# Optimization experiments

Hardware: AMD Instinct MI355X
Metric: run time of the kernel (lower is better)

Reference implementation:

```python
import jax, jax.numpy as jnp
import numpy as np

EPS = 1e-5  # nn.LayerNorm default
H = 16      # n_heads

def _ln(x, s, b):
    m = x.mean(-1, keepdims=True)
    v = x.var(-1, keepdims=True)
    return (x - m) / jnp.sqrt(v + EPS) * s + b


def setup_inputs() -> dict:
    key = jax.random.key(0)
    B, T, D, L, V = 2, 1024, 1024, 6, 32000
    ks = jax.random.split(key, 10)
    def n(k, shape):
        return jax.random.normal(k, shape, dtype=jnp.float32) * 0.02
    return dict(
        x=jax.random.randint(ks[0], (B, T), 0, V),
        tok_emb=n(ks[1], (V, D)),
        pos_emb=n(ks[2], (T, D)),
        Wq=n(ks[3], (L, D, D)), bq=jnp.zeros((L, D), jnp.float32),
        Wk=n(ks[4], (L, D, D)), bk=jnp.zeros((L, D), jnp.float32),
        Wv=n(ks[5], (L, D, D)), bv=jnp.zeros((L, D), jnp.float32),
        ln1_s=jnp.ones((L, D), jnp.float32), ln1_b=jnp.zeros((L, D), jnp.float32),
        W1=n(ks[6], (L, D, 4 * D)), b1=jnp.zeros((L, 4 * D), jnp.float32),
        W2=n(ks[7], (L, 4 * D, D)), b2=jnp.zeros((L, D), jnp.float32),
        ln2_s=jnp.ones((L, D), jnp.float32), ln2_b=jnp.zeros((L, D), jnp.float32),
        Wout=n(ks[8], (D, V)), bout=jnp.zeros((V,), jnp.float32),
    )


def reference(x, tok_emb, pos_emb, Wq, bq, Wk, bk, Wv, bv, ln1_s, ln1_b,
              W1, b1, W2, b2, ln2_s, ln2_b, Wout, bout):
    B, T = x.shape
    D = tok_emb.shape[1]
    hd = D // H
    # embeddings (dropout = identity in eval)
    h = tok_emb[x] + pos_emb[:T]
    # additive causal mask: +1.0 on allowed (tril ones kept), -inf elsewhere,
    # exactly matching torch's tril-ones masked_fill mask
    tril = jnp.tril(jnp.ones((T, T), dtype=h.dtype))
    mask = jnp.where(tril == 0, -jnp.inf, 1.0).astype(h.dtype)
    scale = jnp.asarray(1.0 / np.sqrt(hd), h.dtype)

    def block(h, p):
        wq, bq_, wk, bk_, wv, bv_, l1s, l1b, w1, b1_, w2, b2_, l2s, l2b = p
        def heads(W, b):  # [B,T,D] -> [B,H,T,hd]
            return (h @ W + b).reshape(B, T, H, hd).transpose(0, 2, 1, 3)
        q, k, v = heads(wq, bq_), heads(wk, bk_), heads(wv, bv_)
        s = jnp.einsum('bhqd,bhkd->bhqk', q, k) * scale + mask
        a = jax.nn.softmax(s, axis=-1)
        o = jnp.einsum('bhqk,bhkd->bhqd', a, v).transpose(0, 2, 1, 3).reshape(B, T, D)
        hi = _ln(o + h, l1s, l1b)
        f = jax.nn.relu(hi @ w1 + b1_) @ w2 + b2_
        return _ln(f + hi, l2s, l2b), None

    h, _ = jax.lax.scan(block, h, (Wq, bq, Wk, bk, Wv, bv, ln1_s, ln1_b,
                                   W1, b1, W2, b2, ln2_s, ln2_b))
    return h @ Wout + bout
```

## Files before the change

### kernel.cpp

```cpp
#include <hip/hip_runtime.h>
#include <cstdint>
#include <cstddef>

typedef short bf16x8 __attribute__((ext_vector_type(8)));
typedef float f32x4 __attribute__((ext_vector_type(4)));
typedef unsigned short us4 __attribute__((ext_vector_type(4)));

#define DEV static __device__ __forceinline__

DEV unsigned short f2bf(float f) {
  union { float f; unsigned u; } v; v.f = f;
  unsigned r = v.u + 0x7FFFu + ((v.u >> 16) & 1u);
  return (unsigned short)(r >> 16);
}

DEV void gll16(const void* g, void* l) {
  __builtin_amdgcn_global_load_lds((const __attribute__((address_space(1))) void*)g,
                                   (__attribute__((address_space(3))) void*)l,
                                   16, 0, 0);
}

__global__ __launch_bounds__(256) void embed_kernel(
    const int* __restrict__ x, const float* __restrict__ te,
    const float* __restrict__ pe, float* __restrict__ hf,
    unsigned short* __restrict__ hb) {
  int row = blockIdx.x;
  int t = row & 1023;
  int tok = x[row];
  int tid = threadIdx.x;
  float4 v = ((const float4*)(te + (size_t)tok * 1024))[tid];
  float4 p = ((const float4*)(pe + (size_t)t * 1024))[tid];
  v.x += p.x; v.y += p.y; v.z += p.z; v.w += p.w;
  ((float4*)(hf + (size_t)row * 1024))[tid] = v;
  us4 bv; bv[0] = f2bf(v.x); bv[1] = f2bf(v.y); bv[2] = f2bf(v.z); bv[3] = f2bf(v.w);
  ((us4*)(hb + (size_t)row * 1024))[tid] = bv;
}

__global__ __launch_bounds__(256) void wconv_kernel(
    const float* __restrict__ W, unsigned short* __restrict__ Wt, int K, int N) {
  __shared__ float tile[32][33];
  int n0 = blockIdx.x * 32, k0 = blockIdx.y * 32;
  int tx = threadIdx.x & 31, ty = threadIdx.x >> 5;
#pragma unroll
  for (int i = 0; i < 4; ++i)
    tile[ty * 4 + i][tx] = W[(size_t)(k0 + ty * 4 + i) * N + n0 + tx];
  __syncthreads();
#pragma unroll
  for (int i = 0; i < 4; ++i)
    Wt[(size_t)(n0 + ty * 4 + i) * K + k0 + tx] = f2bf(tile[tx][ty * 4 + i]);
}

__global__ __launch_bounds__(256) void wconv5_kernel(
    const float* __restrict__ Wqf, const float* __restrict__ Wkf,
    const float* __restrict__ Wvf, const float* __restrict__ W1f,
    const float* __restrict__ W2f, unsigned short* __restrict__ wsc) {
  __shared__ float tile[32][33];
  const int bid = blockIdx.x;
  const float* W; unsigned short* Wt; int K, N, b;
  if (bid < 3072) {
    const int s = bid >> 10; b = bid & 1023;
    W = s == 0 ? Wqf : (s == 1 ? Wkf : Wvf);
    Wt = wsc + (size_t)s * 1048576; K = 1024; N = 1024;
  } else if (bid < 7168) {
    b = bid - 3072; W = W1f; Wt = wsc + 3145728; K = 1024; N = 4096;
  } else {
    b = bid - 7168; W = W2f; Wt = wsc + 7340032; K = 4096; N = 1024;
  }
  const int nb = N >> 5;
  const int n0 = (b & (nb - 1)) * 32, k0 = (b / nb) * 32;
  const int tx = threadIdx.x & 31, ty = threadIdx.x >> 5;
#pragma unroll
  for (int i = 0; i < 4; ++i)
    tile[ty * 4 + i][tx] = W[(size_t)(k0 + ty * 4 + i) * N + n0 + tx];
  __syncthreads();
#pragma unroll
  for (int i = 0; i < 4; ++i)
    Wt[(size_t)(n0 + ty * 4 + i) * K + k0 + tx] = f2bf(tile[tx][ty * 4 + i]);
}

template <int EPI>
__global__ __launch_bounds__(512) void gemm5_kernel(
    const unsigned short* __restrict__ A, const unsigned short* __restrict__ Bt,
    const float* __restrict__ bias1, const float* __restrict__ bias2,
    const float* __restrict__ bias3, void* __restrict__ C1,
    void* __restrict__ C2, void* __restrict__ C3,
    int M, int N, int Kstride, int klen, int nbm) {
  constexpr int BM = 256, BN = 128, BK = 64;
  __shared__ unsigned short lA[BM * BK];
  __shared__ unsigned short lB[BN * BK];
  const int tid = threadIdx.x;
  const int wid = tid >> 6, lane = tid & 63;
  const int g = lane >> 4, c = lane & 15;
  const int wm = wid >> 1, wn = wid & 1;

  const int nwg = gridDim.x;
  const int q = nwg >> 3, r = nwg & 7;
  const int xcd = blockIdx.x & 7, jj = blockIdx.x >> 3;
  const int wgid = (xcd < r) ? (xcd * (q + 1) + jj)
                             : (r * (q + 1) + (xcd - r) * q + jj);
  const int bm = (wgid % nbm) * BM;
  const int bn = (wgid / nbm) * BN;
  const int k0 = blockIdx.z * klen;

  f32x4 acc[4][4];
#pragma unroll
  for (int mi = 0; mi < 4; ++mi)
#pragma unroll
    for (int ni = 0; ni < 4; ++ni) acc[mi][ni] = f32x4{0.f, 0.f, 0.f, 0.f};

  for (int kb = 0; kb < klen; kb += BK) {
#pragma unroll
    for (int it = 0; it < 4; ++it) {
      int chunk = it * 512 + tid;
      int row = chunk >> 3, cr = chunk & 7;
      int sc = cr ^ (row & 7);
      gll16(A + (size_t)(bm + row) * Kstride + k0 + kb + sc * 8,
            lA + (size_t)(it * 512 + wid * 64) * 8);
    }
#pragma unroll
    for (int it = 0; it < 2; ++it) {
      int chunk = it * 512 + tid;
      int row = chunk >> 3, cr = chunk & 7;
      int sc = cr ^ (row & 7);
      gll16(Bt + (size_t)(bn + row) * Kstride + k0 + kb + sc * 8,
            lB + (size_t)(it * 512 + wid * 64) * 8);
    }
    __syncthreads();
#pragma unroll
    for (int kk = 0; kk < 2; ++kk) {
      bf16x8 af[4], bfr[4];
#pragma unroll
      for (int mi = 0; mi < 4; ++mi) {
        int row = wm * 64 + mi * 16 + c;
        int ch = (kk * 4 + g) ^ (row & 7);
        af[mi] = *(const bf16x8*)(lA + row * BK + ch * 8);
      }
#pragma unroll
      for (int ni = 0; ni < 4; ++ni) {
        int row = wn * 64 + ni * 16 + c;
        int ch = (kk * 4 + g) ^ (row & 7);
        bfr[ni] = *(const bf16x8*)(lB + row * BK + ch * 8);
      }
#pragma unroll
      for (int mi = 0; mi < 4; ++mi)
#pragma unroll
        for (int ni = 0; ni < 4; ++ni)
          acc[mi][ni] = __builtin_amdgcn_mfma_f32_16x16x32_bf16(
              af[mi], bfr[ni], acc[mi][ni], 0, 0, 0);
    }
    __syncthreads();
  }

  const bool z0 = (blockIdx.z == 0);
#pragma unroll
  for (int mi = 0; mi < 4; ++mi) {
    const int row0 = bm + wm * 64 + mi * 16 + g * 4;
#pragma unroll
    for (int ni = 0; ni < 4; ++ni) {
      const int col = bn + wn * 64 + ni * 16 + c;
      if constexpr (EPI == 0) {
        float* C = (float*)C1 + (size_t)blockIdx.z * M * N;
        const float bv = z0 ? bias1[col] : 0.f;
#pragma unroll
        for (int rr = 0; rr < 4; ++rr)
          C[(size_t)(row0 + rr) * N + col] = acc[mi][ni][rr] + bv;
      } else if constexpr (EPI == 2) {
        const float bv = bias1[col];
#pragma unroll
        for (int rr = 0; rr < 4; ++rr)
          ((unsigned short*)C1)[(size_t)(row0 + rr) * N + col] =
              f2bf(fmaxf(acc[mi][ni][rr] + bv, 0.f));
      } else {
        if (col < 1024) {
          const float bv = bias1[col];
#pragma unroll
          for (int rr = 0; rr < 4; ++rr)
            ((unsigned short*)C1)[(size_t)(row0 + rr) * 1024 + col] =
                f2bf(acc[mi][ni][rr] + bv);
        } else if (col < 2048) {
          const float bv = bias2[col - 1024];
#pragma unroll
          for (int rr = 0; rr < 4; ++rr)
            ((unsigned short*)C2)[(size_t)(row0 + rr) * 1024 + (col - 1024)] =
                f2bf(acc[mi][ni][rr] + bv);
        } else {
          const int cp = col - 2048;
          const float bv = bias3[cp];
          const int hh = cp >> 6, hd = cp & 63;
#pragma unroll
          for (int rr = 0; rr < 4; ++rr) {
            const int row = row0 + rr;
            const int b = row >> 10, t = row & 1023;
            ((unsigned short*)C3)[(size_t)((b * 16 + hh) * 64 + hd) * 1024 + t] =
                f2bf(acc[mi][ni][rr] + bv);
          }
        }
      }
    }
  }
}

__global__ __launch_bounds__(256) void attn_kernel(
    const unsigned short* __restrict__ q, const unsigned short* __restrict__ k,
    const unsigned short* __restrict__ vt, float* __restrict__ o) {
  __shared__ unsigned short lK[128 * 64];
  __shared__ unsigned short lV[64 * 128];
  __shared__ unsigned short lP[4][16 * 128];
  const int tid = threadIdx.x, wid = tid >> 6, lane = tid & 63;
  const int g = lane >> 4, c = lane & 15;
  const int qb = blockIdx.x * 64;
  const int h = blockIdx.y;
  const int b = blockIdx.z;
  const int qw = qb + wid * 16;

  bf16x8 aq[2];
#pragma unroll
  for (int kk = 0; kk < 2; ++kk)
    aq[kk] = *(const bf16x8*)(q + (size_t)(b * 1024 + qw + c) * 1024 + h * 64 + kk * 32 + g * 8);

  float m_run[4], l_run[4];
  f32x4 acc_o[4];
#pragma unroll
  for (int rr = 0; rr < 4; ++rr) { m_run[rr] = -INFINITY; l_run[rr] = 0.f; }
#pragma unroll
  for (int ni = 0; ni < 4; ++ni) acc_o[ni] = f32x4{0.f, 0.f, 0.f, 0.f};

  const int ntiles = (qb >> 7) + 1;
  for (int kt = 0; kt < ntiles; ++kt) {
#pragma unroll
    for (int it = 0; it < 4; ++it) {
      int chunk = it * 256 + tid;
      int row = chunk >> 3, cr = chunk & 7;
      int sc = cr ^ (row & 7);
      gll16(k + (size_t)(b * 1024 + kt * 128 + row) * 1024 + h * 64 + sc * 8,
            lK + (size_t)(it * 256 + wid * 64) * 8);
    }
#pragma unroll
    for (int it = 0; it < 4; ++it) {
      int chunk = it * 256 + tid;
      int row = chunk >> 4, cr = chunk & 15;
      int sc = cr ^ (row & 7);
      gll16(vt + (size_t)((b * 16 + h) * 64 + row) * 1024 + kt * 128 + sc * 8,
            lV + (size_t)(it * 256 + wid * 64) * 8);
    }
    __syncthreads();

    f32x4 accs[8];
#pragma unroll
    for (int ni = 0; ni < 8; ++ni) accs[ni] = f32x4{0.f, 0.f, 0.f, 0.f};
    __builtin_amdgcn_s_setprio(1);
#pragma unroll
    for (int kk = 0; kk < 2; ++kk)
#pragma unroll
      for (int ni = 0; ni < 8; ++ni) {
        int row = ni * 16 + c;
        int ch = (kk * 4 + g) ^ (row & 7);
        bf16x8 kf = *(const bf16x8*)(lK + row * 64 + ch * 8);
        accs[ni] = __builtin_amdgcn_mfma_f32_16x16x32_bf16(aq[kk], kf, accs[ni], 0, 0, 0);
      }
    __builtin_amdgcn_s_setprio(0);

    const bool diag = (kt == ntiles - 1);
    float p[8][4], rowmax[4];
#pragma unroll
    for (int rr = 0; rr < 4; ++rr) rowmax[rr] = -INFINITY;
#pragma unroll
    for (int ni = 0; ni < 8; ++ni)
#pragma unroll
      for (int rr = 0; rr < 4; ++rr) {
        float s = accs[ni][rr] * 0.125f;
        if (diag) {
          int ktok = kt * 128 + ni * 16 + c;
          int qtok = qw + g * 4 + rr;
          if (ktok > qtok) s = -INFINITY;
        }
        p[ni][rr] = s;
        rowmax[rr] = fmaxf(rowmax[rr], s);
      }
#pragma unroll
    for (int mm = 1; mm < 16; mm <<= 1)
#pragma unroll
      for (int rr = 0; rr < 4; ++rr)
        rowmax[rr] = fmaxf(rowmax[rr], __shfl_xor(rowmax[rr], mm, 64));

    float alpha[4];
#pragma unroll
    for (int rr = 0; rr < 4; ++rr) {
      float mn = fmaxf(m_run[rr], rowmax[rr]);
      alpha[rr] = __expf(m_run[rr] - mn);
      m_run[rr] = mn;
    }
#pragma unroll
    for (int ni = 0; ni < 8; ++ni)
#pragma unroll
      for (int rr = 0; rr < 4; ++rr) p[ni][rr] = __expf(p[ni][rr] - m_run[rr]);

    float rowsum[4];
#pragma unroll
    for (int rr = 0; rr < 4; ++rr)
      rowsum[rr] = ((p[0][rr] + p[1][rr]) + (p[2][rr] + p[3][rr])) +
                   ((p[4][rr] + p[5][rr]) + (p[6][rr] + p[7][rr]));
#pragma unroll
    for (int mm = 1; mm < 16; mm <<= 1)
#pragma unroll
      for (int rr = 0; rr < 4; ++rr) rowsum[rr] += __shfl_xor(rowsum[rr], mm, 64);
#pragma unroll
    for (int rr = 0; rr < 4; ++rr) l_run[rr] = l_run[rr] * alpha[rr] + rowsum[rr];
#pragma unroll
    for (int ni = 0; ni < 4; ++ni)
#pragma unroll
      for (int rr = 0; rr < 4; ++rr) acc_o[ni][rr] *= alpha[rr];

#pragma unroll
    for (int ni = 0; ni < 8; ++ni)
#pragma unroll
      for (int rr = 0; rr < 4; ++rr) {
        int qrow = g * 4 + rr;
        int tok = ni * 16 + c;
        int ch = (tok >> 3) ^ (qrow & 7);
        lP[wid][qrow * 128 + ch * 8 + (tok & 7)] = f2bf(p[ni][rr]);
      }

    __builtin_amdgcn_s_setprio(1);
#pragma unroll
    for (int kk = 0; kk < 4; ++kk) {
      int kc = kk * 4 + g;
      int chp = kc ^ (c & 7);
      bf16x8 pa = *(const bf16x8*)(&lP[wid][c * 128 + chp * 8]);
#pragma unroll
      for (int ni = 0; ni < 4; ++ni) {
        int row = ni * 16 + c;
        int ch = kc ^ (row & 7);
        bf16x8 vf = *(const bf16x8*)(lV + row * 128 + ch * 8);
        acc_o[ni] = __builtin_amdgcn_mfma_f32_16x16x32_bf16(pa, vf, acc_o[ni], 0, 0, 0);
      }
    }
    __builtin_amdgcn_s_setprio(0);
    __syncthreads();
  }

#pragma unroll
  for (int ni = 0; ni < 4; ++ni)
#pragma unroll
    for (int rr = 0; rr < 4; ++rr) {
      int row = b * 1024 + qw + g * 4 + rr;
      int col = h * 64 + ni * 16 + c;
      o[(size_t)row * 1024 + col] = acc_o[ni][rr] / l_run[rr];
    }
}

template <int NP>
__global__ __launch_bounds__(256) void ln_add_kernel(
    const float* __restrict__ a1, const float* __restrict__ res,
    const float* __restrict__ s, const float* __restrict__ bb,
    float* __restrict__ out_f, unsigned short* __restrict__ out_b) {
  int row = blockIdx.x, tid = threadIdx.x;
  float4 x = ((const float4*)(a1 + (size_t)row * 1024))[tid];
  float4 rv = ((const float4*)(res + (size_t)row * 1024))[tid];
  x.x += rv.x; x.y += rv.y; x.z += rv.z; x.w += rv.w;
#pragma unroll
  for (int pimg = 1; pimg < NP; ++pimg) {
    float4 x2 = ((const float4*)(a1 + (size_t)pimg * 2097152 + (size_t)row * 1024))[tid];
    x.x += x2.x; x.y += x2.y; x.z += x2.z; x.w += x2.w;
  }
  float sum = x.x + x.y + x.z + x.w;
  float sq = x.x * x.x + x.y * x.y + x.z * x.z + x.w * x.w;
#pragma unroll
  for (int mm = 1; mm < 64; mm <<= 1) {
    sum += __shfl_xor(sum, mm, 64);
    sq += __shfl_xor(sq, mm, 64);
  }
  __shared__ float ssum[4], ssq[4];
  int wid = tid >> 6, lane = tid & 63;
  if (lane == 0) { ssum[wid] = sum; ssq[wid] = sq; }
  __syncthreads();
  sum = ssum[0] + ssum[1] + ssum[2] + ssum[3];
  sq = ssq[0] + ssq[1] + ssq[2] + ssq[3];
  float mean = sum * (1.f / 1024.f);
  float var = sq * (1.f / 1024.f) - mean * mean;
  float rstd = rsqrtf(var + 1e-5f);
  float4 sv = ((const float4*)s)[tid];
  float4 bv = ((const float4*)bb)[tid];
  float4 y;
  y.x = (x.x - mean) * rstd * sv.x + bv.x;
  y.y = (x.y - mean) * rstd * sv.y + bv.y;
  y.z = (x.z - mean) * rstd * sv.z + bv.z;
  y.w = (x.w - mean) * rstd * sv.w + bv.w;
  ((float4*)(out_f + (size_t)row * 1024))[tid] = y;
  us4 ob; ob[0] = f2bf(y.x); ob[1] = f2bf(y.y); ob[2] = f2bf(y.z); ob[3] = f2bf(y.w);
  ((us4*)(out_b + (size_t)row * 1024))[tid] = ob;
}

extern "C" void kernel_launch(void* const* d_in, const int* in_sizes, int n_in,
                              void* d_out, int out_size, void* d_ws, size_t ws_size,
                              hipStream_t stream) {
  const int D = 1024, DFF = 4096, V = 32000, L = 6;
  const int* x = (const int*)d_in[0];
  const float* tok_emb = (const float*)d_in[1];
  const float* pos_emb = (const float*)d_in[2];
  const float* Wq = (const float*)d_in[3];  const float* bq = (const float*)d_in[4];
  const float* Wk = (const float*)d_in[5];  const float* bk = (const float*)d_in[6];
  const float* Wv = (const float*)d_in[7];  const float* bv = (const float*)d_in[8];
  const float* ln1s = (const float*)d_in[9];  const float* ln1b = (const float*)d_in[10];
  const float* W1 = (const float*)d_in[11];  const float* b1 = (const float*)d_in[12];
  const float* W2 = (const float*)d_in[13];  const float* b2 = (const float*)d_in[14];
  const float* ln2s = (const float*)d_in[15]; const float* ln2b = (const float*)d_in[16];
  const float* Wout = (const float*)d_in[17]; const float* bout = (const float*)d_in[18];

  char* ws = (char*)d_ws;
  float* h_res = (float*)(ws + 0);
  float* hi_res = (float*)(ws + 8388608);
  float* tmp = (float*)(ws + 16777216);
  unsigned short* hbf = (unsigned short*)(ws + 25165824);
  unsigned short* qb_ = (unsigned short*)(ws + 29360128);
  unsigned short* kb_ = (unsigned short*)(ws + 33554432);
  unsigned short* vtb = (unsigned short*)(ws + 37748736);
  unsigned short* ffn1 = (unsigned short*)(ws + 41943040);
  unsigned short* wsc = (unsigned short*)(ws + 58720256);
  float* part = (float*)(ws + 58720256 + 25165824);

  embed_kernel<<<2048, 256, 0, stream>>>(x, tok_emb, pos_emb, h_res, hbf);

  for (int l = 0; l < L; ++l) {
    wconv5_kernel<<<11264, 256, 0, stream>>>(
        Wq + (size_t)l * D * D, Wk + (size_t)l * D * D, Wv + (size_t)l * D * D,
        W1 + (size_t)l * D * DFF, W2 + (size_t)l * DFF * D, wsc);
    gemm5_kernel<4><<<192, 512, 0, stream>>>(
        hbf, wsc, bq + l * D, bk + l * D, bv + l * D, qb_, kb_, vtb,
        2048, 3072, D, D, 8);
    attn_kernel<<<dim3(16, 16, 2), 256, 0, stream>>>(qb_, kb_, vtb, tmp);
    ln_add_kernel<1><<<2048, 256, 0, stream>>>(
        tmp, h_res, ln1s + l * D, ln1b + l * D, hi_res, hbf);
    gemm5_kernel<2><<<256, 512, 0, stream>>>(
        hbf, wsc + 3145728, b1 + l * DFF, nullptr, nullptr, ffn1, nullptr, nullptr,
        2048, DFF, D, D, 8);
    gemm5_kernel<0><<<dim3(64, 1, 4), 512, 0, stream>>>(
        ffn1, wsc + 7340032, b2 + l * D, nullptr, nullptr, part, nullptr, nullptr,
        2048, D, DFF, 1024, 8);
    ln_add_kernel<4><<<2048, 256, 0, stream>>>(
        part, hi_res, ln2s + l * D, ln2b + l * D, h_res, hbf);
  }

  wconv_kernel<<<dim3(1000, 32), 256, 0, stream>>>(Wout, wsc, D, V);
  gemm5_kernel<0><<<2000, 512, 0, stream>>>(
      hbf, wsc, bout, nullptr, nullptr, (float*)d_out, nullptr, nullptr,
      2048, V, D, D, 8);
}
```

Before: 1.155 ms.

## Add 256x256 ping-pong GEMM with XCD remap for output projection

Adds a new GEMM kernel with 256x256 tiles, double-buffered LDS loaded via global_load_lds in half-tile stages interleaved with four MFMA quadrants, explicit vmcnt waits and barriers, setprio around MFMA bursts, and an XCD-aware workgroup remapping. It replaces the previous gemm5 launch for the final vocab projection (2048x32000x1024). Larger tiles raise arithmetic intensity and the staged schedule aims to overlap loads with MFMA, at the cost of one workgroup per CU and many barriers.

```diff
diff --git a/kernel.cpp b/kernel.cpp
--- a/kernel.cpp
+++ b/kernel.cpp
@@ -19,6 +19,15 @@
                                    (__attribute__((address_space(3))) void*)l,
                                    16, 0, 0);
 }
+
+template <int N> DEV void waitvm() {
+  if constexpr (N == 0) asm volatile("s_waitcnt vmcnt(0)" ::: "memory");
+  else if constexpr (N == 6) asm volatile("s_waitcnt vmcnt(6)" ::: "memory");
+  else asm volatile("s_waitcnt vmcnt(8)" ::: "memory");
+}
+
+#define SB0 __builtin_amdgcn_sched_barrier(0)
+#define BARR do { SB0; __builtin_amdgcn_s_barrier(); SB0; } while (0)
 
 __global__ __launch_bounds__(256) void embed_kernel(
     const int* __restrict__ x, const float* __restrict__ te,
@@ -198,6 +207,159 @@
       }
     }
   }
+}
+
+template <int BM, int BN, int EPI>
+__global__ __launch_bounds__(512, 1) void gemm8_kernel(
+    const unsigned short* __restrict__ A, const unsigned short* __restrict__ Bt,
+    const float* __restrict__ bias1, void* __restrict__ C1,
+    int M, int N, int K, int nbm) {
+  constexpr int BK = 64;
+  constexpr int MFR = BM / 64;
+  constexpr int NFR = BN / 128;
+  constexpr int IA = BM / 128;
+  constexpr int IB = BN / 128;
+  constexpr int VMW = IA + 2 * IB;
+  __shared__ unsigned short lA[2 * BM * BK];
+  __shared__ unsigned short lB[2 * BN * BK];
+  const int tid = threadIdx.x, wid = tid >> 6, lane = tid & 63;
+  const int g = lane >> 4, c = lane & 15;
+  const int wm = wid >> 2, wn = wid & 3;
+
+  const int nwg = gridDim.x;
+  const int q = nwg >> 3, r = nwg & 7;
+  const int xcd = blockIdx.x & 7, jj = blockIdx.x >> 3;
+  const int wgid = (xcd < r) ? (xcd * (q + 1) + jj)
+                             : (r * (q + 1) + (xcd - r) * q + jj);
+  const int bm = (wgid % nbm) * BM;
+  const int bn = (wgid / nbm) * BN;
+  const int NT = K / BK;
+
+  f32x4 acc[2][MFR][2][NFR];
+#pragma unroll
+  for (int a = 0; a < 2; ++a)
+#pragma unroll
+    for (int mi = 0; mi < MFR; ++mi)
+#pragma unroll
+      for (int b = 0; b < 2; ++b)
+#pragma unroll
+        for (int ni = 0; ni < NFR; ++ni) acc[a][mi][b][ni] = f32x4{0.f, 0.f, 0.f, 0.f};
+
+  bf16x8 af[2][MFR][2];
+  bf16x8 bfr[2][NFR][2];
+
+#define STG_A(tileI, half) do {                                              \
+    const int t_ = (tileI);                                                  \
+    const int kb_ = (t_ < NT ? t_ : NT - 1) * BK;                            \
+    unsigned short* dA_ = lA + (t_ & 1) * (BM * BK);                         \
+    _Pragma("unroll")                                                        \
+    for (int i_ = 0; i_ < IA; ++i_) {                                        \
+      const int chunk_ = (half) * (BM * 4) + i_ * 512 + tid;                 \
+      const int row_ = chunk_ >> 3, cr_ = chunk_ & 7;                        \
+      const int sc_ = cr_ ^ (row_ & 7);                                      \
+      gll16(A + (size_t)(bm + row_) * K + kb_ + sc_ * 8,                     \
+            dA_ + ((half) * (BM * 4) + i_ * 512 + wid * 64) * 8);            \
+    } } while (0)
+
+#define STG_B(tileI, half) do {                                              \
+    const int t_ = (tileI);                                                  \
+    const int kb_ = (t_ < NT ? t_ : NT - 1) * BK;                            \
+    unsigned short* dB_ = lB + (t_ & 1) * (BN * BK);                         \
+    _Pragma("unroll")                                                        \
+    for (int i_ = 0; i_ < IB; ++i_) {                                        \
+      const int chunk_ = (half) * (BN * 4) + i_ * 512 + tid;                 \
+      const int row_ = chunk_ >> 3, cr_ = chunk_ & 7;                        \
+      const int sc_ = cr_ ^ (row_ & 7);                                      \
+      gll16(Bt + (size_t)(bn + row_) * K + kb_ + sc_ * 8,                    \
+            dB_ + ((half) * (BN * 4) + i_ * 512 + wid * 64) * 8);            \
+    } } while (0)
+
+#define RD_A(qm_) do {                                                       \
+    const unsigned short* sA_ = lA + cur * (BM * BK);                        \
+    _Pragma("unroll")                                                        \
+    for (int mi = 0; mi < MFR; ++mi)                                         \
+      _Pragma("unroll")                                                      \
+      for (int kk = 0; kk < 2; ++kk) {                                       \
+        const int row_ = (qm_) * (BM / 2) + wm * (BM / 4) + mi * 16 + c;     \
+        const int ch_ = (kk * 4 + g) ^ (row_ & 7);                           \
+        af[qm_][mi][kk] = *(const bf16x8*)(sA_ + row_ * BK + ch_ * 8);       \
+      } } while (0)
+
+#define RD_B(qn_) do {                                                       \
+    const unsigned short* sB_ = lB + cur * (BN * BK);                        \
+    _Pragma("unroll")                                                        \
+    for (int ni = 0; ni < NFR; ++ni)                                         \
+      _Pragma("unroll")                                                      \
+      for (int kk = 0; kk < 2; ++kk) {                                       \
+        const int row_ = (qn_) * (BN / 2) + wn * (BN / 8) + ni * 16 + c;     \
+        const int ch_ = (kk * 4 + g) ^ (row_ & 7);                           \
+        bfr[qn_][ni][kk] = *(const bf16x8*)(sB_ + row_ * BK + ch_ * 8);      \
+      } } while (0)
+
+#define MFMAQ(qm_, qn_) do {                                                 \
+    __builtin_amdgcn_s_setprio(1);                                           \
+    _Pragma("unroll")                                                        \
+    for (int mi = 0; mi < MFR; ++mi)                                         \
+      _Pragma("unroll")                                                      \
+      for (int ni = 0; ni < NFR; ++ni)                                       \
+        _Pragma("unroll")                                                    \
+        for (int kk = 0; kk < 2; ++kk)                                       \
+          acc[qm_][mi][qn_][ni] = __builtin_amdgcn_mfma_f32_16x16x32_bf16(   \
+              af[qm_][mi][kk], bfr[qn_][ni][kk], acc[qm_][mi][qn_][ni], 0, 0, 0); \
+    __builtin_amdgcn_s_setprio(0);                                           \
+  } while (0)
+
+  STG_A(0, 0); STG_B(0, 0); STG_B(0, 1); STG_A(0, 1);
+  STG_A(1, 0); STG_B(1, 0); STG_B(1, 1);
+  waitvm<VMW>();
+  BARR;
+
+  for (int X = 0; X < NT; ++X) {
+    const int cur = X & 1;
+    RD_A(0); RD_B(0);
+    STG_A(X + 1, 1);
+    BARR;
+    MFMAQ(0, 0);
+    BARR;
+    RD_B(1);
+    STG_A(X + 2, 0);
+    BARR;
+    MFMAQ(0, 1);
+    BARR;
+    RD_A(1);
+    STG_B(X + 2, 0);
+    BARR;
+    MFMAQ(1, 1);
+    BARR;
+    STG_B(X + 2, 1);
+    BARR;
+    MFMAQ(1, 0);
+    waitvm<VMW>();
+    BARR;
+  }
+
+#undef STG_A
+#undef STG_B
+#undef RD_A
+#undef RD_B
+#undef MFMAQ
+
+#pragma unroll
+  for (int qm = 0; qm < 2; ++qm)
+#pragma unroll
+    for (int mi = 0; mi < MFR; ++mi)
+#pragma unroll
+      for (int qn = 0; qn < 2; ++qn)
+#pragma unroll
+        for (int ni = 0; ni < NFR; ++ni) {
+          const int col = bn + qn * (BN / 2) + wn * (BN / 8) + ni * 16 + c;
+          const int row0 = bm + qm * (BM / 2) + wm * (BM / 4) + mi * 16 + g * 4;
+#pragma unroll
+          for (int rr = 0; rr < 4; ++rr) {
+            ((float*)C1)[(size_t)(row0 + rr) * N + col] =
+                acc[qm][mi][qn][ni][rr] + bias1[col];
+          }
+        }
 }
 
 __global__ __launch_bounds__(256) void attn_kernel(
@@ -442,7 +604,6 @@
   }
 
   wconv_kernel<<<dim3(1000, 32), 256, 0, stream>>>(Wout, wsc, D, V);
-  gemm5_kernel<0><<<2000, 512, 0, stream>>>(
-      hbf, wsc, bout, nullptr, nullptr, (float*)d_out, nullptr, nullptr,
-      2048, V, D, D, 8);
-}
+  gemm8_kernel<256, 256, 0><<<1000, 512, 0, stream>>>(
+      hbf, wsc, bout, (float*)d_out, 2048, V, D, 8);
+}
```

Result: slower. 1.191 ms (+3.1%).

## Fuse fp32 weight transpose and bf16 conversion into GEMM B-tile loads

Applied to the files above, without the earlier changes.

Removes the separate wconv kernels, which transposed and converted every layer's weights and the output projection to bf16 in workspace before each GEMM. The GEMM now reads fp32 weights straight from the original row-major layout, converts eight K-values per thread to bf16 in registers, and writes them swizzled into LDS. This avoids the extra write and re-read of the converted weights plus several kernel launches per layer. In exchange, B tiles come through synchronous register loads instead of async global-to-LDS copies. Each weight tile is also fetched in fp32 once per M-block, which relies on L2 to absorb the repeated reads.

```diff
diff --git a/kernel.cpp b/kernel.cpp
--- a/kernel.cpp
+++ b/kernel.cpp
@@ -36,55 +36,15 @@
   ((us4*)(hb + (size_t)row * 1024))[tid] = bv;
 }
 
-__global__ __launch_bounds__(256) void wconv_kernel(
-    const float* __restrict__ W, unsigned short* __restrict__ Wt, int K, int N) {
-  __shared__ float tile[32][33];
-  int n0 = blockIdx.x * 32, k0 = blockIdx.y * 32;
-  int tx = threadIdx.x & 31, ty = threadIdx.x >> 5;
-#pragma unroll
-  for (int i = 0; i < 4; ++i)
-    tile[ty * 4 + i][tx] = W[(size_t)(k0 + ty * 4 + i) * N + n0 + tx];
-  __syncthreads();
-#pragma unroll
-  for (int i = 0; i < 4; ++i)
-    Wt[(size_t)(n0 + ty * 4 + i) * K + k0 + tx] = f2bf(tile[tx][ty * 4 + i]);
-}
-
-__global__ __launch_bounds__(256) void wconv5_kernel(
-    const float* __restrict__ Wqf, const float* __restrict__ Wkf,
-    const float* __restrict__ Wvf, const float* __restrict__ W1f,
-    const float* __restrict__ W2f, unsigned short* __restrict__ wsc) {
-  __shared__ float tile[32][33];
-  const int bid = blockIdx.x;
-  const float* W; unsigned short* Wt; int K, N, b;
-  if (bid < 3072) {
-    const int s = bid >> 10; b = bid & 1023;
-    W = s == 0 ? Wqf : (s == 1 ? Wkf : Wvf);
-    Wt = wsc + (size_t)s * 1048576; K = 1024; N = 1024;
-  } else if (bid < 7168) {
-    b = bid - 3072; W = W1f; Wt = wsc + 3145728; K = 1024; N = 4096;
-  } else {
-    b = bid - 7168; W = W2f; Wt = wsc + 7340032; K = 4096; N = 1024;
-  }
-  const int nb = N >> 5;
-  const int n0 = (b & (nb - 1)) * 32, k0 = (b / nb) * 32;
-  const int tx = threadIdx.x & 31, ty = threadIdx.x >> 5;
-#pragma unroll
-  for (int i = 0; i < 4; ++i)
-    tile[ty * 4 + i][tx] = W[(size_t)(k0 + ty * 4 + i) * N + n0 + tx];
-  __syncthreads();
-#pragma unroll
-  for (int i = 0; i < 4; ++i)
-    Wt[(size_t)(n0 + ty * 4 + i) * K + k0 + tx] = f2bf(tile[tx][ty * 4 + i]);
-}
-
 template <int EPI>
-__global__ __launch_bounds__(512) void gemm5_kernel(
-    const unsigned short* __restrict__ A, const unsigned short* __restrict__ Bt,
+__global__ __launch_bounds__(512) void gemmv_kernel(
+    const unsigned short* __restrict__ A,
+    const float* __restrict__ Wa, const float* __restrict__ Wb,
+    const float* __restrict__ Wc,
     const float* __restrict__ bias1, const float* __restrict__ bias2,
     const float* __restrict__ bias3, void* __restrict__ C1,
     void* __restrict__ C2, void* __restrict__ C3,
-    int M, int N, int Kstride, int klen, int nbm) {
+    int M, int N, int Kstride, int klen, int nbm, int Nw) {
   constexpr int BM = 256, BN = 128, BK = 64;
   __shared__ unsigned short lA[BM * BK];
   __shared__ unsigned short lB[BN * BK];
@@ -102,6 +62,18 @@
   const int bn = (wgid / nbm) * BN;
   const int k0 = blockIdx.z * klen;
 
+  const float* Wsel; int ncol;
+  if constexpr (EPI == 4) {
+    const int seg = bn >> 10;
+    Wsel = seg == 0 ? Wa : (seg == 1 ? Wb : Wc);
+    ncol = bn & 1023;
+  } else {
+    Wsel = Wa; ncol = bn;
+  }
+
+  const int n_ = tid & 127;
+  const int kc0 = (tid >> 7) * 2;
+
   f32x4 acc[4][4];
 #pragma unroll
   for (int mi = 0; mi < 4; ++mi)
@@ -118,12 +90,14 @@
             lA + (size_t)(it * 512 + wid * 64) * 8);
     }
 #pragma unroll
-    for (int it = 0; it < 2; ++it) {
-      int chunk = it * 512 + tid;
-      int row = chunk >> 3, cr = chunk & 7;
-      int sc = cr ^ (row & 7);
-      gll16(Bt + (size_t)(bn + row) * Kstride + k0 + kb + sc * 8,
-            lB + (size_t)(it * 512 + wid * 64) * 8);
+    for (int u = 0; u < 2; ++u) {
+      const int kc = kc0 + u;
+      const float* src = Wsel + (size_t)(k0 + kb + kc * 8) * Nw + ncol + n_;
+      bf16x8 p;
+#pragma unroll
+      for (int j = 0; j < 8; ++j) p[j] = (short)f2bf(src[(size_t)j * Nw]);
+      const int ch = kc ^ (n_ & 7);
+      *(bf16x8*)(lB + n_ * BK + ch * 8) = p;
     }
     __syncthreads();
 #pragma unroll
@@ -416,33 +390,31 @@
   unsigned short* kb_ = (unsigned short*)(ws + 33554432);
   unsigned short* vtb = (unsigned short*)(ws + 37748736);
   unsigned short* ffn1 = (unsigned short*)(ws + 41943040);
-  unsigned short* wsc = (unsigned short*)(ws + 58720256);
-  float* part = (float*)(ws + 58720256 + 25165824);
+  float* part = (float*)(ws + 58720256);
 
   embed_kernel<<<2048, 256, 0, stream>>>(x, tok_emb, pos_emb, h_res, hbf);
 
   for (int l = 0; l < L; ++l) {
-    wconv5_kernel<<<11264, 256, 0, stream>>>(
-        Wq + (size_t)l * D * D, Wk + (size_t)l * D * D, Wv + (size_t)l * D * D,
-        W1 + (size_t)l * D * DFF, W2 + (size_t)l * DFF * D, wsc);
-    gemm5_kernel<4><<<192, 512, 0, stream>>>(
-        hbf, wsc, bq + l * D, bk + l * D, bv + l * D, qb_, kb_, vtb,
-        2048, 3072, D, D, 8);
+    gemmv_kernel<4><<<192, 512, 0, stream>>>(
+        hbf, Wq + (size_t)l * D * D, Wk + (size_t)l * D * D, Wv + (size_t)l * D * D,
+        bq + l * D, bk + l * D, bv + l * D, qb_, kb_, vtb,
+        2048, 3072, D, D, 8, D);
     attn_kernel<<<dim3(16, 16, 2), 256, 0, stream>>>(qb_, kb_, vtb, tmp);
     ln_add_kernel<1><<<2048, 256, 0, stream>>>(
         tmp, h_res, ln1s + l * D, ln1b + l * D, hi_res, hbf);
-    gemm5_kernel<2><<<256, 512, 0, stream>>>(
-        hbf, wsc + 3145728, b1 + l * DFF, nullptr, nullptr, ffn1, nullptr, nullptr,
-        2048, DFF, D, D, 8);
-    gemm5_kernel<0><<<dim3(64, 1, 4), 512, 0, stream>>>(
-        ffn1, wsc + 7340032, b2 + l * D, nullptr, nullptr, part, nullptr, nullptr,
-        2048, D, DFF, 1024, 8);
+    gemmv_kernel<2><<<256, 512, 0, stream>>>(
+        hbf, W1 + (size_t)l * D * DFF, nullptr, nullptr,
+        b1 + l * DFF, nullptr, nullptr, ffn1, nullptr, nullptr,
+        2048, DFF, D, D, 8, DFF);
+    gemmv_kernel<0><<<dim3(64, 1, 4), 512, 0, stream>>>(
+        ffn1, W2 + (size_t)l * DFF * D, nullptr, nullptr,
+        b2 + l * D, nullptr, nullptr, part, nullptr, nullptr,
+        2048, D, DFF, 1024, 8, D);
     ln_add_kernel<4><<<2048, 256, 0, stream>>>(
         part, hi_res, ln2s + l * D, ln2b + l * D, h_res, hbf);
   }
 
-  wconv_kernel<<<dim3(1000, 32), 256, 0, stream>>>(Wout, wsc, D, V);
-  gemm5_kernel<0><<<2000, 512, 0, stream>>>(
-      hbf, wsc, bout, nullptr, nullptr, (float*)d_out, nullptr, nullptr,
-      2048, V, D, D, 8);
-}
+  gemmv_kernel<0><<<2000, 512, 0, stream>>>(
+      hbf, Wout, nullptr, nullptr, bout, nullptr, nullptr,
+      (float*)d_out, nullptr, nullptr, 2048, V, D, D, 8, V);
+}
```

Result: slower. 1.273 ms (+10.2%).
